# Kernel optimization log

Hardware: AMD Instinct MI355X
Metric: run time of the kernel (lower is better)

Reference implementation:

```python
import jax, jax.numpy as jnp
import numpy as np

B, S, DIM = 2, 2048, 4096
NH, NKV, HD = 32, 8, 128
N_REP = NH // NKV


def apply_rope(x, cos, sin):
    # x: [B, S, H, HD]; cos/sin: [S, HD//2]
    xp = x.reshape(*x.shape[:-1], HD // 2, 2)
    xr, xi = xp[..., 0], xp[..., 1]
    c = cos[None, :, None, :]
    s = sin[None, :, None, :]
    orr = xr * c - xi * s
    oi = xr * s + xi * c
    return jnp.stack([orr, oi], axis=-1).reshape(x.shape)


def setup_inputs() -> dict:
    key = jax.random.key(0)
    ks = jax.random.split(key, 8)
    scale = 1.0 / np.sqrt(DIM)
    return {
        "x": jax.random.normal(ks[0], (B, S, DIM), jnp.float32),
        "wq": jax.random.normal(ks[1], (DIM, NH * HD), jnp.float32) * scale,
        "wk": jax.random.normal(ks[2], (DIM, NKV * HD), jnp.float32) * scale,
        "wv": jax.random.normal(ks[3], (DIM, NKV * HD), jnp.float32) * scale,
        "wo": jax.random.normal(ks[4], (NH * HD, DIM), jnp.float32) * scale,
        "freqs_cos": jnp.cos(jnp.arange(S, dtype=jnp.float32)[:, None]
                             * (1.0 / (10000.0 ** (jnp.arange(0, HD, 2, dtype=jnp.float32) / HD)))[None, :]),
        "freqs_sin": jnp.sin(jnp.arange(S, dtype=jnp.float32)[:, None]
                             * (1.0 / (10000.0 ** (jnp.arange(0, HD, 2, dtype=jnp.float32) / HD)))[None, :]),
        "cache_k": jnp.zeros((B, S, NKV, HD), jnp.float32),
        "cache_v": jnp.zeros((B, S, NKV, HD), jnp.float32),
        "start_pos": 0,
    }


def reference(x, wq, wk, wv, wo, freqs_cos, freqs_sin, cache_k, cache_v, start_pos):
    b, s, _ = x.shape
    xq = (x @ wq).reshape(b, s, NH, HD)
    xk = (x @ wk).reshape(b, s, NKV, HD)
    xv = (x @ wv).reshape(b, s, NKV, HD)
    xq = apply_rope(xq, freqs_cos, freqs_sin)
    xk = apply_rope(xk, freqs_cos, freqs_sin)
    # KV-cache append (start_pos is a static Python int)
    cache_k = jax.lax.dynamic_update_slice(cache_k, xk, (0, start_pos, 0, 0))
    cache_v = jax.lax.dynamic_update_slice(cache_v, xv, (0, start_pos, 0, 0))
    t = start_pos + s
    keys = cache_k[:, :t]    # [B, T, NKV, HD]
    values = cache_v[:, :t]
    # GQA attention without materializing repeated KV
    q = xq.transpose(0, 2, 1, 3).reshape(b, NKV, N_REP, s, HD)  # [B, K, R, S, HD]
    k = keys.transpose(0, 2, 1, 3)    # [B, K, T, HD]
    v = values.transpose(0, 2, 1, 3)  # [B, K, T, HD]
    inv_sqrt = 1.0 / np.sqrt(HD)
    scores = jnp.einsum('bkrsd,bktd->bkrst', q, k * inv_sqrt)  # keys scaled, as in original
    probs = jax.nn.softmax(scores.astype(jnp.float32), axis=-1).astype(q.dtype)
    out = jnp.einsum('bkrst,bktd->bkrsd', probs, v)  # [B, K, R, S, HD]
    out = out.reshape(b, NH, s, HD).transpose(0, 2, 1, 3).reshape(b, s, NH * HD)
    return out @ wo
```

## Files before the change

### kernel.cpp

```cpp
#include <hip/hip_runtime.h>
#include <cstdint>
#include <cstddef>

#define B_    2
#define S_    2048
#define DIM_  4096
#define NH_   32
#define NKV_  8
#define HD_   128

typedef short bf16x8 __attribute__((ext_vector_type(8)));
typedef float f32x4  __attribute__((ext_vector_type(4)));

__device__ __forceinline__ short f2bf(float x) {
  unsigned u = __builtin_bit_cast(unsigned, x);
  u += 0x7fffu + ((u >> 16) & 1u);
  return (short)(u >> 16);
}
__device__ __forceinline__ float bf2f(short s) {
  unsigned u = ((unsigned)(unsigned short)s) << 16;
  return __builtin_bit_cast(float, u);
}

#define GLDS(gp, lp) __builtin_amdgcn_global_load_lds( \
    (const __attribute__((address_space(1))) void*)(gp), \
    (__attribute__((address_space(3))) void*)(lp), 16, 0, 0)

__global__ void cast_x(const float* __restrict__ in, short* __restrict__ out) {
  int i = (blockIdx.x * 256 + threadIdx.x) * 4;
  const float4 v = *(const float4*)(in + i);
  short4 o;
  o.x = f2bf(v.x); o.y = f2bf(v.y); o.z = f2bf(v.z); o.w = f2bf(v.w);
  *(short4*)(out + i) = o;
}

__global__ void tcast(const float* __restrict__ W, short* __restrict__ Wt, int K, int N) {
  __shared__ float t[32][33];
  int tid = threadIdx.x;
  int r = tid >> 3, c4 = (tid & 7) << 2;
  int n0 = blockIdx.x << 5, k0 = blockIdx.y << 5;
  const float4 v = *(const float4*)(W + (size_t)(k0 + r) * N + n0 + c4);
  t[r][c4] = v.x; t[r][c4 + 1] = v.y; t[r][c4 + 2] = v.z; t[r][c4 + 3] = v.w;
  __syncthreads();
  short4 o;
  o.x = f2bf(t[c4][r]); o.y = f2bf(t[c4 + 1][r]);
  o.z = f2bf(t[c4 + 2][r]); o.w = f2bf(t[c4 + 3][r]);
  *(short4*)(Wt + (size_t)(n0 + r) * K + k0 + c4) = o;
}

template <int OUT_BF16>
__global__ __launch_bounds__(256) void gemm_bt(const short* __restrict__ A,
                                               const short* __restrict__ Bt,
                                               float* __restrict__ Cf,
                                               short* __restrict__ Cb,
                                               int M, int N, int K) {
  __shared__ __align__(16) short As[128 * 32];
  __shared__ __align__(16) short Bs[128 * 32];
  const int tid = threadIdx.x;
  const int wave = tid >> 6, lane = tid & 63;
  const int quad = lane >> 4, l16 = lane & 15;
  const int bm = blockIdx.y << 7, bn = blockIdx.x << 7;
  const int wm = (wave >> 1) << 6, wn = (wave & 1) << 6;

  f32x4 acc[4][4];
  for (int i = 0; i < 4; ++i)
    for (int j = 0; j < 4; ++j)
      for (int r = 0; r < 4; ++r) acc[i][j][r] = 0.f;

  const int sw = quad ^ ((l16 >> 1) & 3);

  for (int k0 = 0; k0 < K; k0 += 32) {
    __syncthreads();
#pragma unroll
    for (int rr = 0; rr < 2; ++rr) {
      const int idb = rr * 256 + wave * 64;
      const int id = idb + lane;
      const int ar = id >> 2;
      const int ac = (id & 3) ^ ((ar >> 1) & 3);
      GLDS(A  + (size_t)(bm + ar) * K + k0 + ac * 8, As + idb * 8);
      GLDS(Bt + (size_t)(bn + ar) * K + k0 + ac * 8, Bs + idb * 8);
    }
    __syncthreads();

    bf16x8 af[4], bfr[4];
#pragma unroll
    for (int i = 0; i < 4; ++i)
      af[i] = *(const bf16x8*)(As + ((wm + i * 16 + l16) * 4 + sw) * 8);
#pragma unroll
    for (int i = 0; i < 4; ++i)
      bfr[i] = *(const bf16x8*)(Bs + ((wn + i * 16 + l16) * 4 + sw) * 8);
#pragma unroll
    for (int mi = 0; mi < 4; ++mi)
#pragma unroll
      for (int ni = 0; ni < 4; ++ni)
        acc[mi][ni] = __builtin_amdgcn_mfma_f32_16x16x32_bf16(af[mi], bfr[ni],
                                                              acc[mi][ni], 0, 0, 0);
  }
#pragma unroll
  for (int mi = 0; mi < 4; ++mi)
#pragma unroll
    for (int ni = 0; ni < 4; ++ni)
#pragma unroll
      for (int r = 0; r < 4; ++r) {
        int row = bm + wm + mi * 16 + quad * 4 + r;
        int col = bn + wn + ni * 16 + l16;
        size_t off = (size_t)row * N + col;
        if (OUT_BF16) Cb[off] = f2bf(acc[mi][ni][r]);
        else          Cf[off] = acc[mi][ni][r];
      }
}

#define QSCALE 0.12751745444105413f
__global__ void rope_pack_q(const short* __restrict__ xq, const float* __restrict__ fc,
                            const float* __restrict__ fs, short* __restrict__ qp) {
  int i = blockIdx.x * 256 + threadIdx.x;
  int d = i & 63; int t = i >> 6;
  int h = t & (NH_ - 1); t >>= 5;
  int s = t & (S_ - 1);  int b = t >> 11;
  size_t src = ((size_t)((b * S_ + s) * NH_ + h)) * HD_ + 2 * d;
  unsigned rv = *(const unsigned*)(xq + src);
  float xr = bf2f((short)(rv & 0xffff)), xi = bf2f((short)(rv >> 16));
  float c = fc[s * 64 + d], sn = fs[s * 64 + d];
  float orr = (xr * c - xi * sn) * QSCALE, oi = (xr * sn + xi * c) * QSCALE;
  size_t dst = ((size_t)((b * NH_ + h) * S_ + s)) * HD_ + 2 * d;
  unsigned pv = (unsigned)(unsigned short)f2bf(orr) |
                ((unsigned)(unsigned short)f2bf(oi) << 16);
  *(unsigned*)(qp + dst) = pv;
}

__global__ void rope_pack_k(const short* __restrict__ xk, const float* __restrict__ fc,
                            const float* __restrict__ fs, short* __restrict__ kp) {
  int i = blockIdx.x * 256 + threadIdx.x;
  int d = i & 63; int t = i >> 6;
  int kh = t & (NKV_ - 1); t >>= 3;
  int s = t & (S_ - 1); int b = t >> 11;
  size_t src = ((size_t)((b * S_ + s) * NKV_ + kh)) * HD_ + 2 * d;
  unsigned rv = *(const unsigned*)(xk + src);
  float xr = bf2f((short)(rv & 0xffff)), xi = bf2f((short)(rv >> 16));
  float c = fc[s * 64 + d], sn = fs[s * 64 + d];
  float orr = xr * c - xi * sn, oi = xr * sn + xi * c;
  size_t dst = ((size_t)((b * NKV_ + kh) * S_ + s)) * HD_ + 2 * d;
  unsigned pv = (unsigned)(unsigned short)f2bf(orr) |
                ((unsigned)(unsigned short)f2bf(oi) << 16);
  *(unsigned*)(kp + dst) = pv;
}

__global__ void pack_v(const short* __restrict__ xv, short* __restrict__ vt) {
  int i = blockIdx.x * 256 + threadIdx.x;
  int p = i & (S_ - 1); int t = i >> 11;
  int hd = t & (HD_ - 1); t >>= 7;
  int kh = t & (NKV_ - 1); int b = t >> 3;
  vt[i] = xv[((size_t)(b * S_ + p) * NKV_ + kh) * HD_ + hd];
}

__global__ __launch_bounds__(256) void attn(const short* __restrict__ Qp,
                                            const short* __restrict__ Kp,
                                            const short* __restrict__ Vt,
                                            short* __restrict__ AO) {
  __shared__ __align__(16) short Ks[64 * 128];
  __shared__ __align__(16) short Vs[128 * 64];
  __shared__ __align__(16) short Ps[4][16 * 64];
  const int tid = threadIdx.x, wave = tid >> 6, lane = tid & 63;
  const int quad = lane >> 4, l16 = lane & 15;
  const int qt = blockIdx.x, h = blockIdx.y, b = blockIdx.z;
  const int kh = h >> 2;
  const short* Qh = Qp + ((size_t)(b * NH_ + h) * S_) * HD_;
  const short* Kh = Kp + ((size_t)(b * NKV_ + kh) * S_) * HD_;
  const short* Vh = Vt + ((size_t)(b * NKV_ + kh) * HD_) * S_;

  const int qrow = qt * 64 + wave * 16 + l16;
  bf16x8 qf[4];
#pragma unroll
  for (int ks = 0; ks < 4; ++ks)
    qf[ks] = *(const bf16x8*)(Qh + (size_t)qrow * HD_ + ks * 32 + quad * 8);

  f32x4 o[8];
  for (int i = 0; i < 8; ++i)
    for (int r = 0; r < 4; ++r) o[i][r] = 0.f;
  float lsum = 0.f;
  const int l7 = l16 & 7;
  short* Pw = &Ps[wave][0];

  for (int t0 = 0; t0 < S_; t0 += 64) {
    __syncthreads();
#pragma unroll
    for (int rr = 0; rr < 4; ++rr) {
      int idb = rr * 256 + wave * 64;
      int id = idb + lane;
      int kr = id >> 4, kc = (id & 15) ^ (kr & 7);
      GLDS(Kh + (size_t)(t0 + kr) * HD_ + kc * 8, Ks + idb * 8);
      int vr = id >> 3, vc = (id & 7) ^ (vr & 7);
      GLDS(Vh + (size_t)vr * S_ + t0 + vc * 8, Vs + idb * 8);
    }
    __syncthreads();

#pragma unroll
    for (int kb = 0; kb < 4; ++kb) {
      f32x4 a;
      for (int r = 0; r < 4; ++r) a[r] = 0.f;
#pragma unroll
      for (int ks = 0; ks < 4; ++ks) {
        bf16x8 kf = *(const bf16x8*)(Ks + ((kb * 16 + l16) * 16 +
                                           ((ks * 4 + quad) ^ l7)) * 8);
        a = __builtin_amdgcn_mfma_f32_16x16x32_bf16(kf, qf[ks], a, 0, 0, 0);
      }
      float p0 = __builtin_amdgcn_exp2f(a[0]);
      float p1 = __builtin_amdgcn_exp2f(a[1]);
      float p2 = __builtin_amdgcn_exp2f(a[2]);
      float p3 = __builtin_amdgcn_exp2f(a[3]);
      lsum += (p0 + p1) + (p2 + p3);
      unsigned w0 = (unsigned)(unsigned short)f2bf(p0) |
                    ((unsigned)(unsigned short)f2bf(p1) << 16);
      unsigned w1 = (unsigned)(unsigned short)f2bf(p2) |
                    ((unsigned)(unsigned short)f2bf(p3) << 16);
      int c16 = (kb * 2 + (quad >> 1)) ^ l7;
      uint2 wv; wv.x = w0; wv.y = w1;
      *(uint2*)(Pw + l16 * 64 + c16 * 8 + (quad & 1) * 4) = wv;
    }

#pragma unroll
    for (int ks = 0; ks < 2; ++ks) {
      bf16x8 pf = *(const bf16x8*)(Pw + (l16 * 8 + ((ks * 4 + quad) ^ l7)) * 8);
#pragma unroll
      for (int ob = 0; ob < 8; ++ob) {
        bf16x8 vf = *(const bf16x8*)(Vs + ((ob * 16 + l16) * 8 +
                                           ((ks * 4 + quad) ^ l7)) * 8);
        o[ob] = __builtin_amdgcn_mfma_f32_16x16x32_bf16(vf, pf, o[ob], 0, 0, 0);
      }
    }
  }

  lsum += __shfl_xor(lsum, 16, 64);
  lsum += __shfl_xor(lsum, 32, 64);
  float linv = __builtin_amdgcn_rcpf(lsum);
#pragma unroll
  for (int ob = 0; ob < 8; ++ob) {
    short4 s4;
    s4.x = f2bf(o[ob][0] * linv);
    s4.y = f2bf(o[ob][1] * linv);
    s4.z = f2bf(o[ob][2] * linv);
    s4.w = f2bf(o[ob][3] * linv);
    *(short4*)(AO + ((size_t)b * S_ + qrow) * (NH_ * HD_) + h * HD_ +
               ob * 16 + quad * 4) = s4;
  }
}

extern "C" void kernel_launch(void* const* d_in, const int* in_sizes, int n_in,
                              void* d_out, int out_size, void* d_ws, size_t ws_size,
                              hipStream_t stream) {
  (void)in_sizes; (void)n_in; (void)out_size; (void)ws_size;
  const float* x  = (const float*)d_in[0];
  const float* wq = (const float*)d_in[1];
  const float* wk = (const float*)d_in[2];
  const float* wv = (const float*)d_in[3];
  const float* wo = (const float*)d_in[4];
  const float* fc = (const float*)d_in[5];
  const float* fs = (const float*)d_in[6];
  float* out = (float*)d_out;

  char* ws = (char*)d_ws;
  short* xb  = (short*)(ws + 0);
  short* wqt = (short*)(ws + 33554432);
  short* wkt = (short*)(ws + 67108864);
  short* wvt = (short*)(ws + 75497472);
  short* wot = (short*)(ws + 83886080);
  short* xq  = (short*)(ws + 117440512);
  short* xk  = (short*)(ws + 150994944);
  short* xv  = (short*)(ws + 159383552);
  short* kp  = (short*)(ws + 167772160);
  short* vt  = (short*)(ws + 176160768);
  short* qp = xb;
  short* ao = xq;

  cast_x<<<16384, 256, 0, stream>>>(x, xb);
  tcast<<<dim3(128, 128), 256, 0, stream>>>(wq, wqt, 4096, 4096);
  tcast<<<dim3(32, 128),  256, 0, stream>>>(wk, wkt, 4096, 1024);
  tcast<<<dim3(32, 128),  256, 0, stream>>>(wv, wvt, 4096, 1024);
  tcast<<<dim3(128, 128), 256, 0, stream>>>(wo, wot, 4096, 4096);

  gemm_bt<1><<<dim3(32, 32), 256, 0, stream>>>(xb, wqt, nullptr, xq, 4096, 4096, 4096);
  gemm_bt<1><<<dim3(8, 32),  256, 0, stream>>>(xb, wkt, nullptr, xk, 4096, 1024, 4096);
  gemm_bt<1><<<dim3(8, 32),  256, 0, stream>>>(xb, wvt, nullptr, xv, 4096, 1024, 4096);

  rope_pack_q<<<32768, 256, 0, stream>>>(xq, fc, fs, qp);
  rope_pack_k<<<8192,  256, 0, stream>>>(xk, fc, fs, kp);
  pack_v<<<16384, 256, 0, stream>>>(xv, vt);

  attn<<<dim3(32, 32, 2), 256, 0, stream>>>(qp, kp, vt, ao);

  gemm_bt<0><<<dim3(32, 32), 256, 0, stream>>>(ao, wot, out, nullptr, 4096, 4096, 4096);
}
```

Baseline: 1.051 ms.

## Add 256x256-tile 8-wave pipelined GEMM for Q and output projections

```diff
diff --git a/kernel.cpp b/kernel.cpp
--- a/kernel.cpp
+++ b/kernel.cpp
@@ -108,6 +108,140 @@
         if (OUT_BF16) Cb[off] = f2bf(acc[mi][ni][r]);
         else          Cf[off] = acc[mi][ni][r];
       }
+}
+
+#define STAGE_HALF(G, row0, k0, Sdst) do { \
+  _Pragma("unroll") \
+  for (int rr_ = 0; rr_ < 2; ++rr_) { \
+    const int idb_ = rr_ * 512 + wave * 64; \
+    const int id_ = idb_ + lane; \
+    const int r_ = id_ >> 3, c_ = id_ & 7; \
+    GLDS((G) + (size_t)((row0) + r_) * 4096 + (k0) + ((c_ ^ (r_ & 7)) * 8), \
+         (Sdst) + idb_ * 8); \
+  } \
+} while (0)
+
+#define PHASE(QM, QN, STAGE_BLOCK, TAIL_BLOCK) do { \
+  bf16x8 af_[4][2], bq_[2][2]; \
+  _Pragma("unroll") \
+  for (int mi = 0; mi < 4; ++mi) { \
+    _Pragma("unroll") \
+    for (int ks = 0; ks < 2; ++ks) \
+      af_[mi][ks] = *(const bf16x8*)(Ac + ((QM) * 128 + wr * 64 + mi * 16 + l16) * 64 \
+                                        + ((ks * 4 + quad) ^ l7s) * 8); \
+  } \
+  _Pragma("unroll") \
+  for (int ni = 0; ni < 2; ++ni) { \
+    _Pragma("unroll") \
+    for (int ks = 0; ks < 2; ++ks) \
+      bq_[ni][ks] = *(const bf16x8*)(Bc + ((QN) * 128 + wc * 32 + ni * 16 + l16) * 64 \
+                                        + ((ks * 4 + quad) ^ l7s) * 8); \
+  } \
+  STAGE_BLOCK \
+  __builtin_amdgcn_s_barrier(); \
+  asm volatile("s_waitcnt lgkmcnt(0)" ::: "memory"); \
+  __builtin_amdgcn_sched_barrier(0); \
+  __builtin_amdgcn_s_setprio(1); \
+  _Pragma("unroll") \
+  for (int mi = 0; mi < 4; ++mi) { \
+    _Pragma("unroll") \
+    for (int ni = 0; ni < 2; ++ni) { \
+      acc[QM][QN][mi][ni] = __builtin_amdgcn_mfma_f32_16x16x32_bf16( \
+          af_[mi][0], bq_[ni][0], acc[QM][QN][mi][ni], 0, 0, 0); \
+      acc[QM][QN][mi][ni] = __builtin_amdgcn_mfma_f32_16x16x32_bf16( \
+          af_[mi][1], bq_[ni][1], acc[QM][QN][mi][ni], 0, 0, 0); \
+    } \
+  } \
+  __builtin_amdgcn_s_setprio(0); \
+  TAIL_BLOCK \
+  __builtin_amdgcn_sched_barrier(0); \
+  __builtin_amdgcn_s_barrier(); \
+} while (0)
+
+template <int OUT_BF16>
+__global__ __launch_bounds__(512, 2) void gemm256(const short* __restrict__ A,
+                                                  const short* __restrict__ Bt,
+                                                  float* __restrict__ Cf,
+                                                  short* __restrict__ Cb,
+                                                  int N) {
+  __shared__ __align__(16) short As[2][256 * 64];
+  __shared__ __align__(16) short Bs[2][256 * 64];
+  const int tid = threadIdx.x;
+  const int wave = tid >> 6, lane = tid & 63;
+  const int quad = lane >> 4, l16 = lane & 15, l7s = l16 & 7;
+  const int wr = wave >> 2, wc = wave & 3;
+  const int bm = blockIdx.y << 8, bn = blockIdx.x << 8;
+
+  f32x4 acc[2][2][4][2];
+#pragma unroll
+  for (int a = 0; a < 2; ++a)
+#pragma unroll
+    for (int b = 0; b < 2; ++b)
+#pragma unroll
+      for (int c = 0; c < 4; ++c)
+#pragma unroll
+        for (int d = 0; d < 2; ++d)
+#pragma unroll
+          for (int r = 0; r < 4; ++r) acc[a][b][c][d][r] = 0.f;
+
+  STAGE_HALF(A,  bm,       0,  &As[0][0]);
+  STAGE_HALF(Bt, bn,       0,  &Bs[0][0]);
+  STAGE_HALF(A,  bm + 128, 0,  &As[0][8192]);
+  STAGE_HALF(Bt, bn + 128, 0,  &Bs[0][8192]);
+  STAGE_HALF(A,  bm,       64, &As[1][0]);
+  STAGE_HALF(Bt, bn + 128, 64, &Bs[1][8192]);
+  asm volatile("s_waitcnt vmcnt(4)" ::: "memory");
+  __builtin_amdgcn_s_barrier();
+
+#pragma clang loop unroll(disable)
+  for (int t = 0; t < 62; ++t) {
+    const int cur = t & 1;
+    short* Ac = &As[cur][0];
+    short* Bc = &Bs[cur][0];
+    short* An = &As[cur ^ 1][0];
+    short* Bn = &Bs[cur ^ 1][0];
+    const int kt1 = (t + 1) << 6, kt2 = (t + 2) << 6;
+    PHASE(0, 0, STAGE_HALF(A, bm + 128, kt1, An + 8192); STAGE_HALF(Bt, bn, kt1, Bn);, ;);
+    PHASE(0, 1, ;, ;);
+    PHASE(1, 1, STAGE_HALF(A, bm, kt2, Ac);, ;);
+    PHASE(1, 0, STAGE_HALF(Bt, bn + 128, kt2, Bc + 8192);,
+          asm volatile("s_waitcnt vmcnt(4)" ::: "memory"););
+  }
+  {
+    short* Ac = &As[0][0];
+    short* Bc = &Bs[0][0];
+    short* An = &As[1][0];
+    short* Bn = &Bs[1][0];
+    PHASE(0, 0, STAGE_HALF(A, bm + 128, 4032, An + 8192); STAGE_HALF(Bt, bn, 4032, Bn);, ;);
+    PHASE(0, 1, ;, ;);
+    PHASE(1, 1, ;, ;);
+    PHASE(1, 0, ;, asm volatile("s_waitcnt vmcnt(0)" ::: "memory"););
+  }
+  {
+    short* Ac = &As[1][0];
+    short* Bc = &Bs[1][0];
+    PHASE(0, 0, ;, ;);
+    PHASE(0, 1, ;, ;);
+    PHASE(1, 1, ;, ;);
+    PHASE(1, 0, ;, ;);
+  }
+
+#pragma unroll
+  for (int qm = 0; qm < 2; ++qm)
+#pragma unroll
+    for (int qn = 0; qn < 2; ++qn)
+#pragma unroll
+      for (int mi = 0; mi < 4; ++mi)
+#pragma unroll
+        for (int ni = 0; ni < 2; ++ni)
+#pragma unroll
+          for (int r = 0; r < 4; ++r) {
+            int row = bm + qm * 128 + wr * 64 + mi * 16 + quad * 4 + r;
+            int col = bn + qn * 128 + wc * 32 + ni * 16 + l16;
+            size_t off = (size_t)row * N + col;
+            if (OUT_BF16) Cb[off] = f2bf(acc[qm][qn][mi][ni][r]);
+            else          Cf[off] = acc[qm][qn][mi][ni][r];
+          }
 }
 
 #define QSCALE 0.12751745444105413f
@@ -278,7 +412,7 @@
   tcast<<<dim3(32, 128),  256, 0, stream>>>(wv, wvt, 4096, 1024);
   tcast<<<dim3(128, 128), 256, 0, stream>>>(wo, wot, 4096, 4096);
 
-  gemm_bt<1><<<dim3(32, 32), 256, 0, stream>>>(xb, wqt, nullptr, xq, 4096, 4096, 4096);
+  gemm256<1><<<dim3(16, 16), 512, 0, stream>>>(xb, wqt, nullptr, xq, 4096);
   gemm_bt<1><<<dim3(8, 32),  256, 0, stream>>>(xb, wkt, nullptr, xk, 4096, 1024, 4096);
   gemm_bt<1><<<dim3(8, 32),  256, 0, stream>>>(xb, wvt, nullptr, xv, 4096, 1024, 4096);
 
@@ -288,5 +422,5 @@
 
   attn<<<dim3(32, 32, 2), 256, 0, stream>>>(qp, kp, vt, ao);
 
-  gemm_bt<0><<<dim3(32, 32), 256, 0, stream>>>(ao, wot, out, nullptr, 4096, 4096, 4096);
-}
+  gemm256<0><<<dim3(16, 16), 512, 0, stream>>>(ao, wot, out, nullptr, 4096);
+}
```

After: 979.2 us. -6.9%, faster.
